# Optimization experiments

Hardware: AMD Instinct MI355X
Metric: run time of the kernel (lower is better)

## Reference

```python
import jax, jax.numpy as jnp
import numpy as np

N_NODES = 100000
N_EDGES = 1600000
D = 64
N_LAYERS = 5  # hops=4 -> hops+1 GraphConv layers


def setup_inputs() -> dict:
    key = jax.random.key(0)
    k1, k2, k3, k4, k5, k6 = jax.random.split(key, 6)
    x = jax.random.normal(k1, (N_NODES, D), dtype=jnp.float32)
    edge_index = jax.random.randint(k2, (2, N_EDGES), 0, N_NODES, dtype=jnp.int64)
    edge_weight = jax.random.uniform(k3, (N_EDGES,), dtype=jnp.float32)
    # Per-layer params (all dims are 64 so we can stack): PyG GraphConv has
    # lin_rel (with bias) applied to the aggregated messages and lin_root
    # (no bias) applied to the node's own features.
    scale = 1.0 / np.sqrt(D)
    W_rel = jax.random.normal(k4, (N_LAYERS, D, D), dtype=jnp.float32) * scale
    b_rel = jnp.zeros((N_LAYERS, D), dtype=jnp.float32)
    W_root = jax.random.normal(k5, (N_LAYERS, D, D), dtype=jnp.float32) * scale
    return {"x": x, "edge_index": edge_index, "edge_weight": edge_weight,
            "W_rel": W_rel, "b_rel": b_rel, "W_root": W_root}


def _graph_conv(x, src, dst, edge_weight, W_rel_i, b_rel_i, W_root_i):
    # message: x_j * w_e ; aggregate: scatter-add onto destination nodes
    msg = x[src] * edge_weight[:, None]               # [E, D] gather
    agg = jax.ops.segment_sum(msg, dst, num_segments=N_NODES)  # [N, D] scatter
    return agg @ W_rel_i + b_rel_i + x @ W_root_i


def reference(x, edge_index, edge_weight, W_rel, b_rel, W_root):
    src, dst = edge_index[0], edge_index[1]
    h = x
    for i in range(N_LAYERS - 1):
        h = _graph_conv(h, src, dst, edge_weight, W_rel[i], b_rel[i], W_root[i])
        h = jax.nn.relu(h)
    h = _graph_conv(h, src, dst, edge_weight, W_rel[-1], b_rel[-1], W_root[-1])
    return h
```

## Files before the change

kernel.cpp:

```cpp
#include <hip/hip_runtime.h>

#define N_NODES 100000
#define N_EDGES 1600000
#define D 64
#define N_LAYERS 5
#define FB 1000
#define BN 100
#define NX 8
#define BCAP_X 320
#define BCAP 2048
#define BIN_BLOCKS 512
#define BIN_THREADS 512
#define BIN_CHUNK 3125

typedef unsigned short u16;
typedef unsigned long long u64;
typedef __attribute__((ext_vector_type(8))) short bf16x8;
typedef __attribute__((ext_vector_type(4))) float f32x4;

__device__ __forceinline__ float bf2f(u16 u) {
    union { unsigned int i; float f; } v;
    v.i = ((unsigned int)u) << 16;
    return v.f;
}
__device__ __forceinline__ u16 f2bf(float f) {
    union { float f; unsigned int i; } v;
    v.f = f;
    unsigned int r = v.i + 0x7FFFu + ((v.i >> 16) & 1u);
    return (u16)(r >> 16);
}
__device__ __forceinline__ float bf2f_lo(unsigned int pk) {
    union { unsigned int i; float f; } v;
    v.i = pk << 16;
    return v.f;
}
__device__ __forceinline__ float bf2f_hi(unsigned int pk) {
    union { unsigned int i; float f; } v;
    v.i = pk & 0xFFFF0000u;
    return v.f;
}


__global__ __launch_bounds__(1024) void initcur_kernel(int* __restrict__ fcur)
{
    int i = blockIdx.x * 1024 + threadIdx.x;
    if (i < NX * FB) fcur[i] = i * BCAP_X;
}

__global__ __launch_bounds__(BIN_THREADS) void bin_kernel(
    const int* __restrict__ src, const int* __restrict__ dst,
    const float* __restrict__ ew, int* __restrict__ fcur,
    u64* __restrict__ stag)
{
    __shared__ int hc[FB];
    const int xbase = (blockIdx.x & (NX - 1)) * FB;
    for (int b = threadIdx.x; b < FB; b += BIN_THREADS) hc[b] = 0;
    __syncthreads();
    const int e0 = blockIdx.x * BIN_CHUNK;
    for (int e = e0 + threadIdx.x; e < e0 + BIN_CHUNK; e += BIN_THREADS) {
        int d = dst[e];
        atomicAdd(&hc[d / BN], 1);
    }
    __syncthreads();
    for (int b = threadIdx.x; b < FB; b += BIN_THREADS) {
        int c = hc[b];
        if (c) hc[b] = atomicAdd(&fcur[xbase + b], c);
    }
    __syncthreads();
    for (int e = e0 + threadIdx.x; e < e0 + BIN_CHUNK; e += BIN_THREADS) {
        int d = dst[e];
        int b = d / BN;
        int pos = atomicAdd(&hc[b], 1);
        int s   = __builtin_nontemporal_load(&src[e]);
        float w = __builtin_nontemporal_load(&ew[e]);
        unsigned int pk = (unsigned int)((d - b * BN) << 17) | (unsigned int)s;
        u64 rec = ((u64)(unsigned int)__float_as_int(w) << 32) | pk;
        stag[pos] = rec;
    }
}

__global__ __launch_bounds__(1024) void fscan_kernel(
    const int* __restrict__ fcur, int* __restrict__ fbase,
    int* __restrict__ rowptr)
{
    __shared__ int s[1024];
    int t = threadIdx.x;
    int v = 0;
    if (t < FB) {
        #pragma unroll
        for (int x = 0; x < NX; ++x) {
            int cell = x * FB + t;
            v += fcur[cell] - cell * BCAP_X;
        }
    }
    s[t] = v;
    __syncthreads();
    for (int off = 1; off < 1024; off <<= 1) {
        int u = (t >= off) ? s[t - off] : 0;
        __syncthreads();
        s[t] += u;
        __syncthreads();
    }
    if (t < FB) fbase[t] = s[t] - v;
    if (t == FB - 1) {
        fbase[FB] = s[t];
        rowptr[N_NODES] = s[t];
    }
}

__global__ __launch_bounds__(256) void sort_kernel(
    const u64* __restrict__ stag, const int* __restrict__ fcur,
    const int* __restrict__ fbase, int* __restrict__ rowptr,
    int2* __restrict__ edges)
{
    __shared__ u64 ls[BCAP];
    __shared__ int cnt[BN];
    __shared__ int cur[BN];
    __shared__ int sc[128];
    const int b = blockIdx.x;
    const int base = fbase[b];
    const int t = threadIdx.x;
    for (int i = t; i < BN; i += 256) cnt[i] = 0;
    __syncthreads();
    int ofs = 0;
    #pragma unroll
    for (int x = 0; x < NX; ++x) {
        int cell = x * FB + b;
        int sz = fcur[cell] - cell * BCAP_X;
        const u64* sp = stag + (size_t)cell * BCAP_X;
        for (int i = t; i < sz; i += 256) {
            u64 r = __builtin_nontemporal_load(&sp[i]);
            ls[ofs + i] = r;
            atomicAdd(&cnt[((unsigned int)r) >> 17], 1);
        }
        ofs += sz;
    }
    const int size = ofs;
    __syncthreads();
    if (t < 128) sc[t] = (t < BN) ? cnt[t] : 0;
    __syncthreads();
    for (int off = 1; off < 128; off <<= 1) {
        int u = 0;
        if (t < 128 && t >= off) u = sc[t - off];
        __syncthreads();
        if (t < 128) sc[t] += u;
        __syncthreads();
    }
    if (t < BN) {
        int excl = sc[t] - cnt[t];
        rowptr[b * BN + t] = base + excl;
        cur[t] = excl;
    }
    __syncthreads();
    for (int i = t; i < size; i += 256) {
        u64 r = ls[i];
        unsigned int lo = (unsigned int)r;
        int dloc = lo >> 17;
        int rank = atomicAdd(&cur[dloc], 1);
        edges[base + rank] = make_int2((int)(lo & 0x1FFFFu),
                                       (int)(unsigned int)(r >> 32));
    }
}

__global__ __launch_bounds__(256) void f2bf_kernel(
    const float* __restrict__ in, u16* __restrict__ out)
{
    int i = blockIdx.x * 256 + threadIdx.x;
    if (i >= (N_NODES * D) / 4) return;
    float4 v = ((const float4*)in)[i];
    ushort4 o;
    o.x = f2bf(v.x); o.y = f2bf(v.y); o.z = f2bf(v.z); o.w = f2bf(v.w);
    ((ushort4*)out)[i] = o;
}

__global__ __launch_bounds__(256) void wprep_kernel(
    const float* __restrict__ Wrel, const float* __restrict__ Wroot,
    u16* __restrict__ W2T)
{
    int i = blockIdx.x * 256 + threadIdx.x;
    if (i >= N_LAYERS * 64 * 128) return;
    int l = i / (64 * 128);
    int rem = i % (64 * 128);
    int n = rem >> 7;
    int k = rem & 127;
    float v = (k < 64) ? Wrel[l * 4096 + k * 64 + n]
                       : Wroot[l * 4096 + (k - 64) * 64 + n];
    W2T[i] = f2bf(v);
}

__global__ __launch_bounds__(256) void layer_kernel(
    const u16* __restrict__ hin, const int* __restrict__ rowptr,
    const int2* __restrict__ edges, const u16* __restrict__ W2T,
    const float* __restrict__ brel,
    u16* __restrict__ hout_bf, float* __restrict__ hout_f32, int relu)
{
    __shared__ u16 aggs[4][16][64];
    const int wave = threadIdx.x >> 6;
    const int lane = threadIdx.x & 63;
    const int nb16 = blockIdx.x * 64 + wave * 16;
    const int sl   = lane & 31;
    const int half = lane >> 5;
    u16* wtile = &aggs[wave][0][0];

    for (int t = 0; t < 8; ++t) {
        int nl = 2 * t + half;
        int node = nb16 + nl;
        float acc0 = 0.f, acc1 = 0.f;
        if (node < N_NODES) {
            int b = rowptr[node];
            int e = rowptr[node + 1];
            for (int base = b; base < e; base += 32) {
                int cnt = min(32, e - base);
                int idx = 0;
                float wv = 0.f;
                if (sl < cnt) {
                    int2 p = edges[base + sl];
                    idx = p.x;
                    wv = __int_as_float(p.y);
                }
                int j = 0;
                for (; j + 8 <= cnt; j += 8) {
                    int s0 = __shfl(idx, j + 0, 32), s1 = __shfl(idx, j + 1, 32);
                    int s2 = __shfl(idx, j + 2, 32), s3 = __shfl(idx, j + 3, 32);
                    int s4 = __shfl(idx, j + 4, 32), s5 = __shfl(idx, j + 5, 32);
                    int s6 = __shfl(idx, j + 6, 32), s7 = __shfl(idx, j + 7, 32);
                    float w0 = __shfl(wv, j + 0, 32), w1 = __shfl(wv, j + 1, 32);
                    float w2 = __shfl(wv, j + 2, 32), w3 = __shfl(wv, j + 3, 32);
                    float w4 = __shfl(wv, j + 4, 32), w5 = __shfl(wv, j + 5, 32);
                    float w6 = __shfl(wv, j + 6, 32), w7 = __shfl(wv, j + 7, 32);
                    unsigned int p0 = *(const unsigned int*)(hin + ((size_t)s0 << 6) + sl * 2);
                    unsigned int p1 = *(const unsigned int*)(hin + ((size_t)s1 << 6) + sl * 2);
                    unsigned int p2 = *(const unsigned int*)(hin + ((size_t)s2 << 6) + sl * 2);
                    unsigned int p3 = *(const unsigned int*)(hin + ((size_t)s3 << 6) + sl * 2);
                    unsigned int p4 = *(const unsigned int*)(hin + ((size_t)s4 << 6) + sl * 2);
                    unsigned int p5 = *(const unsigned int*)(hin + ((size_t)s5 << 6) + sl * 2);
                    unsigned int p6 = *(const unsigned int*)(hin + ((size_t)s6 << 6) + sl * 2);
                    unsigned int p7 = *(const unsigned int*)(hin + ((size_t)s7 << 6) + sl * 2);
                    acc0 += bf2f_lo(p0) * w0 + bf2f_lo(p1) * w1
                          + bf2f_lo(p2) * w2 + bf2f_lo(p3) * w3
                          + bf2f_lo(p4) * w4 + bf2f_lo(p5) * w5
                          + bf2f_lo(p6) * w6 + bf2f_lo(p7) * w7;
                    acc1 += bf2f_hi(p0) * w0 + bf2f_hi(p1) * w1
                          + bf2f_hi(p2) * w2 + bf2f_hi(p3) * w3
                          + bf2f_hi(p4) * w4 + bf2f_hi(p5) * w5
                          + bf2f_hi(p6) * w6 + bf2f_hi(p7) * w7;
                }
                for (; j < cnt; ++j) {
                    int s = __shfl(idx, j, 32);
                    float w = __shfl(wv, j, 32);
                    unsigned int pk = *(const unsigned int*)(hin + ((size_t)s << 6) + sl * 2);
                    acc0 += bf2f_lo(pk) * w;
                    acc1 += bf2f_hi(pk) * w;
                }
            }
        }
        int u16idx = (nl << 6) | ((sl * 2) ^ ((nl & 7) << 3));
        unsigned int o = ((unsigned int)f2bf(acc1) << 16) | f2bf(acc0);
        *(unsigned int*)(wtile + u16idx) = o;
    }

    const int m = lane & 15;
    const int q = lane >> 4;

    bf16x8 a[4];
    {
        int r0 = (m << 6) | ((q * 8) ^ ((m & 7) << 3));
        int r1 = (m << 6) | ((32 + q * 8) ^ ((m & 7) << 3));
        a[0] = *(const bf16x8*)(wtile + r0);
        a[1] = *(const bf16x8*)(wtile + r1);
    }
    int anode = nb16 + m;
    size_t rowa = (size_t)((anode < N_NODES) ? anode : 0) << 6;
    a[2] = *(const bf16x8*)(hin + rowa + q * 8);
    a[3] = *(const bf16x8*)(hin + rowa + 32 + q * 8);

    bf16x8 bfr[4][4];
    #pragma unroll
    for (int nt = 0; nt < 4; ++nt)
        #pragma unroll
        for (int kk = 0; kk < 4; ++kk)
            bfr[nt][kk] = *(const bf16x8*)(W2T + (size_t)(nt * 16 + m) * 128
                                           + kk * 32 + q * 8);

    f32x4 acc[4];
    #pragma unroll
    for (int nt = 0; nt < 4; ++nt) {
        float bv = brel[nt * 16 + m];
        acc[nt] = (f32x4){bv, bv, bv, bv};
    }

    #pragma unroll
    for (int kk = 0; kk < 4; ++kk)
        #pragma unroll
        for (int nt = 0; nt < 4; ++nt)
            acc[nt] = __builtin_amdgcn_mfma_f32_16x16x32_bf16(
                a[kk], bfr[nt][kk], acc[nt], 0, 0, 0);

    #pragma unroll
    for (int nt = 0; nt < 4; ++nt)
        #pragma unroll
        for (int r = 0; r < 4; ++r) {
            int n2 = nb16 + q * 4 + r;
            if (n2 < N_NODES) {
                float v = acc[nt][r];
                if (relu) v = fmaxf(v, 0.f);
                int dim = nt * 16 + m;
                if (hout_f32) hout_f32[(size_t)n2 * 64 + dim] = v;
                else          hout_bf [(size_t)n2 * 64 + dim] = f2bf(v);
            }
        }
}

extern "C" void kernel_launch(void* const* d_in, const int* in_sizes, int n_in,
                              void* d_out, int out_size, void* d_ws, size_t ws_size,
                              hipStream_t stream)
{
    const float* x     = (const float*)d_in[0];
    const int*   ei    = (const int*)d_in[1];
    const float* ew    = (const float*)d_in[2];
    const float* Wrel  = (const float*)d_in[3];
    const float* brel  = (const float*)d_in[4];
    const float* Wroot = (const float*)d_in[5];
    float* out = (float*)d_out;

    const int* src = ei;
    const int* dst = ei + N_EDGES;

    const size_t featb_bytes = (size_t)N_NODES * D * 2;
    char* ws = (char*)d_ws;
    size_t off = 0;
    u16*  hb     = (u16*)(ws + off);  off += featb_bytes;
    u16*  hb2    = (u16*)(ws + off);  off += featb_bytes;
    u16*  W2T    = (u16*)(ws + off);  off += (size_t)N_LAYERS * 64 * 128 * 2;
    int*  rowptr = (int*)(ws + off);  off += 400016;
    int*  fcur   = (int*)(ws + off);  off += NX * FB * 4;
    int*  fbase  = (int*)(ws + off);  off += (FB + 1) * 4 + 60;
    int2* edges  = (int2*)(ws + off); off += (size_t)N_EDGES * 8;

    u64* stag = (u64*)ws;

    u16* hbuf[2] = {hb, hb2};

    const int cblocks = (N_NODES * D / 4 + 255) / 256;
    const int wblocks = (N_LAYERS * 64 * 128 + 255) / 256;
    const int lblocks = (N_NODES + 63) / 64;

    initcur_kernel<<<8, 1024, 0, stream>>>(fcur);
    bin_kernel<<<BIN_BLOCKS, BIN_THREADS, 0, stream>>>(src, dst, ew, fcur, stag);
    fscan_kernel<<<1, 1024, 0, stream>>>(fcur, fbase, rowptr);
    sort_kernel<<<FB, 256, 0, stream>>>(stag, fcur, fbase, rowptr, edges);
    f2bf_kernel<<<cblocks, 256, 0, stream>>>(x, hb);
    wprep_kernel<<<wblocks, 256, 0, stream>>>(Wrel, Wroot, W2T);

    for (int layer = 0; layer < N_LAYERS; ++layer) {
        int last = (layer == N_LAYERS - 1);
        layer_kernel<<<lblocks, 256, 0, stream>>>(
            hbuf[layer & 1], rowptr, edges,
            W2T + (size_t)layer * 64 * 128,
            brel + (size_t)layer * D,
            last ? nullptr : hbuf[(layer + 1) & 1],
            last ? out : nullptr,
            last ? 0 : 1);
    }
}
```

Before: 472.5 us.

## Restructure layer kernel to 16 nodes per 512-thread block with split MFMA

Each block now handles 16 nodes with 8 waves. Every half-wave aggregates one node's neighbours in parallel, where before each wave looped over 8 pairs of nodes. After a block barrier, four waves each compute one 16-column output tile with MFMA, which also cuts the B-fragment registers per wave. The aim is more latency-hiding parallelism in the gather phase. The cost is an extra __syncthreads, four idle waves during the matmul, and removed bounds checks that rely on N_NODES being divisible by 16.

```diff
diff --git a/kernel.cpp b/kernel.cpp
--- a/kernel.cpp
+++ b/kernel.cpp
@@ -188,127 +188,114 @@
     W2T[i] = f2bf(v);
 }
 
-__global__ __launch_bounds__(256) void layer_kernel(
+__global__ __launch_bounds__(512) void layer_kernel(
     const u16* __restrict__ hin, const int* __restrict__ rowptr,
     const int2* __restrict__ edges, const u16* __restrict__ W2T,
     const float* __restrict__ brel,
     u16* __restrict__ hout_bf, float* __restrict__ hout_f32, int relu)
 {
-    __shared__ u16 aggs[4][16][64];
+    __shared__ u16 aggs[16][64];
     const int wave = threadIdx.x >> 6;
     const int lane = threadIdx.x & 63;
-    const int nb16 = blockIdx.x * 64 + wave * 16;
+    const int nb16 = blockIdx.x * 16;
     const int sl   = lane & 31;
     const int half = lane >> 5;
-    u16* wtile = &aggs[wave][0][0];
-
-    for (int t = 0; t < 8; ++t) {
-        int nl = 2 * t + half;
+
+    {
+        int nl = 2 * wave + half;
         int node = nb16 + nl;
         float acc0 = 0.f, acc1 = 0.f;
-        if (node < N_NODES) {
-            int b = rowptr[node];
-            int e = rowptr[node + 1];
-            for (int base = b; base < e; base += 32) {
-                int cnt = min(32, e - base);
-                int idx = 0;
-                float wv = 0.f;
-                if (sl < cnt) {
-                    int2 p = edges[base + sl];
-                    idx = p.x;
-                    wv = __int_as_float(p.y);
-                }
-                int j = 0;
-                for (; j + 8 <= cnt; j += 8) {
-                    int s0 = __shfl(idx, j + 0, 32), s1 = __shfl(idx, j + 1, 32);
-                    int s2 = __shfl(idx, j + 2, 32), s3 = __shfl(idx, j + 3, 32);
-                    int s4 = __shfl(idx, j + 4, 32), s5 = __shfl(idx, j + 5, 32);
-                    int s6 = __shfl(idx, j + 6, 32), s7 = __shfl(idx, j + 7, 32);
-                    float w0 = __shfl(wv, j + 0, 32), w1 = __shfl(wv, j + 1, 32);
-                    float w2 = __shfl(wv, j + 2, 32), w3 = __shfl(wv, j + 3, 32);
-                    float w4 = __shfl(wv, j + 4, 32), w5 = __shfl(wv, j + 5, 32);
-                    float w6 = __shfl(wv, j + 6, 32), w7 = __shfl(wv, j + 7, 32);
-                    unsigned int p0 = *(const unsigned int*)(hin + ((size_t)s0 << 6) + sl * 2);
-                    unsigned int p1 = *(const unsigned int*)(hin + ((size_t)s1 << 6) + sl * 2);
-                    unsigned int p2 = *(const unsigned int*)(hin + ((size_t)s2 << 6) + sl * 2);
-                    unsigned int p3 = *(const unsigned int*)(hin + ((size_t)s3 << 6) + sl * 2);
-                    unsigned int p4 = *(const unsigned int*)(hin + ((size_t)s4 << 6) + sl * 2);
-                    unsigned int p5 = *(const unsigned int*)(hin + ((size_t)s5 << 6) + sl * 2);
-                    unsigned int p6 = *(const unsigned int*)(hin + ((size_t)s6 << 6) + sl * 2);
-                    unsigned int p7 = *(const unsigned int*)(hin + ((size_t)s7 << 6) + sl * 2);
-                    acc0 += bf2f_lo(p0) * w0 + bf2f_lo(p1) * w1
-                          + bf2f_lo(p2) * w2 + bf2f_lo(p3) * w3
-                          + bf2f_lo(p4) * w4 + bf2f_lo(p5) * w5
-                          + bf2f_lo(p6) * w6 + bf2f_lo(p7) * w7;
-                    acc1 += bf2f_hi(p0) * w0 + bf2f_hi(p1) * w1
-                          + bf2f_hi(p2) * w2 + bf2f_hi(p3) * w3
-                          + bf2f_hi(p4) * w4 + bf2f_hi(p5) * w5
-                          + bf2f_hi(p6) * w6 + bf2f_hi(p7) * w7;
-                }
-                for (; j < cnt; ++j) {
-                    int s = __shfl(idx, j, 32);
-                    float w = __shfl(wv, j, 32);
-                    unsigned int pk = *(const unsigned int*)(hin + ((size_t)s << 6) + sl * 2);
-                    acc0 += bf2f_lo(pk) * w;
-                    acc1 += bf2f_hi(pk) * w;
-                }
+        int b = rowptr[node];
+        int e = rowptr[node + 1];
+        for (int base = b; base < e; base += 32) {
+            int cnt = min(32, e - base);
+            int idx = 0;
+            float wv = 0.f;
+            if (sl < cnt) {
+                int2 p = edges[base + sl];
+                idx = p.x;
+                wv = __int_as_float(p.y);
+            }
+            int j = 0;
+            for (; j + 8 <= cnt; j += 8) {
+                int s0 = __shfl(idx, j + 0, 32), s1 = __shfl(idx, j + 1, 32);
+                int s2 = __shfl(idx, j + 2, 32), s3 = __shfl(idx, j + 3, 32);
+                int s4 = __shfl(idx, j + 4, 32), s5 = __shfl(idx, j + 5, 32);
+                int s6 = __shfl(idx, j + 6, 32), s7 = __shfl(idx, j + 7, 32);
+                float w0 = __shfl(wv, j + 0, 32), w1 = __shfl(wv, j + 1, 32);
+                float w2 = __shfl(wv, j + 2, 32), w3 = __shfl(wv, j + 3, 32);
+                float w4 = __shfl(wv, j + 4, 32), w5 = __shfl(wv, j + 5, 32);
+                float w6 = __shfl(wv, j + 6, 32), w7 = __shfl(wv, j + 7, 32);
+                unsigned int p0 = *(const unsigned int*)(hin + ((size_t)s0 << 6) + sl * 2);
+                unsigned int p1 = *(const unsigned int*)(hin + ((size_t)s1 << 6) + sl * 2);
+                unsigned int p2 = *(const unsigned int*)(hin + ((size_t)s2 << 6) + sl * 2);
+                unsigned int p3 = *(const unsigned int*)(hin + ((size_t)s3 << 6) + sl * 2);
+                unsigned int p4 = *(const unsigned int*)(hin + ((size_t)s4 << 6) + sl * 2);
+                unsigned int p5 = *(const unsigned int*)(hin + ((size_t)s5 << 6) + sl * 2);
+                unsigned int p6 = *(const unsigned int*)(hin + ((size_t)s6 << 6) + sl * 2);
+                unsigned int p7 = *(const unsigned int*)(hin + ((size_t)s7 << 6) + sl * 2);
+                acc0 += bf2f_lo(p0) * w0 + bf2f_lo(p1) * w1
+                      + bf2f_lo(p2) * w2 + bf2f_lo(p3) * w3
+                      + bf2f_lo(p4) * w4 + bf2f_lo(p5) * w5
+                      + bf2f_lo(p6) * w6 + bf2f_lo(p7) * w7;
+                acc1 += bf2f_hi(p0) * w0 + bf2f_hi(p1) * w1
+                      + bf2f_hi(p2) * w2 + bf2f_hi(p3) * w3
+                      + bf2f_hi(p4) * w4 + bf2f_hi(p5) * w5
+                      + bf2f_hi(p6) * w6 + bf2f_hi(p7) * w7;
+            }
+            for (; j < cnt; ++j) {
+                int s = __shfl(idx, j, 32);
+                float w = __shfl(wv, j, 32);
+                unsigned int pk = *(const unsigned int*)(hin + ((size_t)s << 6) + sl * 2);
+                acc0 += bf2f_lo(pk) * w;
+                acc1 += bf2f_hi(pk) * w;
             }
         }
         int u16idx = (nl << 6) | ((sl * 2) ^ ((nl & 7) << 3));
         unsigned int o = ((unsigned int)f2bf(acc1) << 16) | f2bf(acc0);
-        *(unsigned int*)(wtile + u16idx) = o;
-    }
-
-    const int m = lane & 15;
-    const int q = lane >> 4;
-
-    bf16x8 a[4];
-    {
-        int r0 = (m << 6) | ((q * 8) ^ ((m & 7) << 3));
-        int r1 = (m << 6) | ((32 + q * 8) ^ ((m & 7) << 3));
-        a[0] = *(const bf16x8*)(wtile + r0);
-        a[1] = *(const bf16x8*)(wtile + r1);
-    }
-    int anode = nb16 + m;
-    size_t rowa = (size_t)((anode < N_NODES) ? anode : 0) << 6;
-    a[2] = *(const bf16x8*)(hin + rowa + q * 8);
-    a[3] = *(const bf16x8*)(hin + rowa + 32 + q * 8);
-
-    bf16x8 bfr[4][4];
-    #pragma unroll
-    for (int nt = 0; nt < 4; ++nt)
+        *(unsigned int*)(&aggs[0][0] + u16idx) = o;
+    }
+    __syncthreads();
+
+    if (wave < 4) {
+        const int nt = wave;
+        const int m = lane & 15;
+        const int q = lane >> 4;
+
+        bf16x8 a[4];
+        {
+            int r0 = (m << 6) | ((q * 8) ^ ((m & 7) << 3));
+            int r1 = (m << 6) | ((32 + q * 8) ^ ((m & 7) << 3));
+            a[0] = *(const bf16x8*)(&aggs[0][0] + r0);
+            a[1] = *(const bf16x8*)(&aggs[0][0] + r1);
+        }
+        size_t rowa = (size_t)(nb16 + m) << 6;
+        a[2] = *(const bf16x8*)(hin + rowa + q * 8);
+        a[3] = *(const bf16x8*)(hin + rowa + 32 + q * 8);
+
+        bf16x8 bfr[4];
         #pragma unroll
         for (int kk = 0; kk < 4; ++kk)
-            bfr[nt][kk] = *(const bf16x8*)(W2T + (size_t)(nt * 16 + m) * 128
-                                           + kk * 32 + q * 8);
-
-    f32x4 acc[4];
-    #pragma unroll
-    for (int nt = 0; nt < 4; ++nt) {
+            bfr[kk] = *(const bf16x8*)(W2T + (size_t)(nt * 16 + m) * 128
+                                       + kk * 32 + q * 8);
+
         float bv = brel[nt * 16 + m];
-        acc[nt] = (f32x4){bv, bv, bv, bv};
-    }
-
-    #pragma unroll
-    for (int kk = 0; kk < 4; ++kk)
+        f32x4 acc = (f32x4){bv, bv, bv, bv};
         #pragma unroll
-        for (int nt = 0; nt < 4; ++nt)
-            acc[nt] = __builtin_amdgcn_mfma_f32_16x16x32_bf16(
-                a[kk], bfr[nt][kk], acc[nt], 0, 0, 0);
-
-    #pragma unroll
-    for (int nt = 0; nt < 4; ++nt)
+        for (int kk = 0; kk < 4; ++kk)
+            acc = __builtin_amdgcn_mfma_f32_16x16x32_bf16(a[kk], bfr[kk],
+                                                          acc, 0, 0, 0);
+
         #pragma unroll
         for (int r = 0; r < 4; ++r) {
             int n2 = nb16 + q * 4 + r;
-            if (n2 < N_NODES) {
-                float v = acc[nt][r];
-                if (relu) v = fmaxf(v, 0.f);
-                int dim = nt * 16 + m;
-                if (hout_f32) hout_f32[(size_t)n2 * 64 + dim] = v;
-                else          hout_bf [(size_t)n2 * 64 + dim] = f2bf(v);
-            }
-        }
+            float v = acc[r];
+            if (relu) v = fmaxf(v, 0.f);
+            int dim = nt * 16 + m;
+            if (hout_f32) hout_f32[(size_t)n2 * 64 + dim] = v;
+            else          hout_bf [(size_t)n2 * 64 + dim] = f2bf(v);
+        }
+    }
 }
 
 extern "C" void kernel_launch(void* const* d_in, const int* in_sizes, int n_in,
@@ -343,7 +330,7 @@
 
     const int cblocks = (N_NODES * D / 4 + 255) / 256;
     const int wblocks = (N_LAYERS * 64 * 128 + 255) / 256;
-    const int lblocks = (N_NODES + 63) / 64;
+    const int lblocks = N_NODES / 16;
 
     initcur_kernel<<<8, 1024, 0, stream>>>(fcur);
     bin_kernel<<<BIN_BLOCKS, BIN_THREADS, 0, stream>>>(src, dst, ew, fcur, stag);
@@ -354,7 +341,7 @@
 
     for (int layer = 0; layer < N_LAYERS; ++layer) {
         int last = (layer == N_LAYERS - 1);
-        layer_kernel<<<lblocks, 256, 0, stream>>>(
+        layer_kernel<<<lblocks, 512, 0, stream>>>(
             hbuf[layer & 1], rowptr, edges,
             W2T + (size_t)layer * 64 * 128,
             brel + (size_t)layer * D,
```

Result: faster. 397.2 us (-16.0%).
